# Performance work log

Hardware: AMD Instinct MI355X
Metric: run time of the kernel (lower is better)

Reference implementation:

```python
import jax, jax.numpy as jnp
import numpy as np
from jax import lax

D_MODEL = 768
D_INNER = 1536   # expand * d_model
D_STATE = 16
D_CONV = 4
DT_RANK = 48     # ceil(768/16)
BATCH, SEQLEN = 2, 1024


def silu(x):
    return x * jax.nn.sigmoid(x)


def causal_conv1d(x, w, b):
    # x: (B, L, d)  w: (d, K) depthwise  b: (d,)
    # matches torch Conv1d(groups=d, padding=K-1)[..., :L]
    K = w.shape[1]
    L = x.shape[1]
    xp = jnp.pad(x, ((0, 0), (K - 1, 0), (0, 0)))
    out = b
    for k in range(K):
        out = out + xp[:, k:k + L, :] * w[:, k]
    return out


def mamba_branch(xz, conv_w, conv_b, x_proj_w, dt_proj_w, dt_bias, A_log, D):
    # xz: (B, L, 2*d_inner); faithful to mamba_inner_fn_no_out_proj
    x, z = jnp.split(xz, 2, axis=-1)
    x = silu(causal_conv1d(x, conv_w, conv_b))
    x_dbl = x @ x_proj_w.T                                  # (B,L,dt_rank+2N)
    dt, Bc, Cc = jnp.split(x_dbl, [DT_RANK, DT_RANK + D_STATE], axis=-1)
    delta = jax.nn.softplus(dt @ dt_proj_w.T + dt_bias)     # (B,L,d)
    A = -jnp.exp(A_log)                                     # (d,N)
    dA = jnp.exp(delta[..., None] * A)                      # (B,L,d,N)
    dBx = (delta * x)[..., None] * Bc[:, :, None, :]        # (B,L,d,N)

    def step(h, inp):
        da, dbx = inp
        h = da * h + dbx
        return h, h

    h0 = jnp.zeros((x.shape[0], x.shape[2], D_STATE), x.dtype)
    _, hs = lax.scan(step, h0, (jnp.swapaxes(dA, 0, 1), jnp.swapaxes(dBx, 0, 1)))
    y = jnp.einsum('lbdn,bln->bld', hs, Cc) + x * D         # (B,L,d)
    return y * silu(z)


def setup_inputs() -> dict:
    key = jax.random.key(0)
    ks = jax.random.split(key, 16)
    d, dm, n, r, K = D_INNER, D_MODEL, D_STATE, DT_RANK, D_CONV
    A_log = jnp.log(jnp.broadcast_to(jnp.arange(1, n + 1, dtype=jnp.float32), (d, n)))
    # faithful dt bias init: inverse-softplus of log-uniform dt in [1e-3, 1e-1]
    def dt_bias(k):
        dt = jnp.exp(jax.random.uniform(k, (d,)) * (np.log(0.1) - np.log(0.001)) + np.log(0.001))
        dt = jnp.clip(dt, 1e-4)
        return dt + jnp.log(-jnp.expm1(-dt))
    return {
        'hidden_states': jax.random.normal(ks[0], (BATCH, SEQLEN, dm), jnp.float32),
        'in_proj_w': jax.random.normal(ks[1], (2 * d, dm), jnp.float32) / np.sqrt(dm),
        'conv_w': jax.random.normal(ks[2], (d, K), jnp.float32) / np.sqrt(K),
        'conv_b': jax.random.normal(ks[3], (d,), jnp.float32) * 0.02,
        'x_proj_w': jax.random.normal(ks[4], (r + 2 * n, d), jnp.float32) / np.sqrt(d),
        'dt_proj_w': jax.random.uniform(ks[5], (d, r), jnp.float32, -r ** -0.5, r ** -0.5),
        'dt_proj_b': dt_bias(ks[6]),
        'A_log': A_log,
        'D': jnp.ones((d,), jnp.float32),
        'conv_w_b': jax.random.normal(ks[7], (d, K), jnp.float32) / np.sqrt(K),
        'conv_b_b': jax.random.normal(ks[8], (d,), jnp.float32) * 0.02,
        'x_proj_w_b': jax.random.normal(ks[9], (r + 2 * n, d), jnp.float32) / np.sqrt(d),
        'dt_proj_w_b': jax.random.uniform(ks[10], (d, r), jnp.float32, -r ** -0.5, r ** -0.5),
        'dt_proj_b_b': dt_bias(ks[11]),
        'A_b_log': A_log,
        'D_b': jnp.ones((d,), jnp.float32),
        'out_proj_w': jax.random.normal(ks[12], (dm, d), jnp.float32) / np.sqrt(d),
    }


def reference(hidden_states, in_proj_w, conv_w, conv_b, x_proj_w, dt_proj_w, dt_proj_b,
              A_log, D, conv_w_b, conv_b_b, x_proj_w_b, dt_proj_w_b, dt_proj_b_b,
              A_b_log, D_b, out_proj_w):
    # bimamba v2: forward scan + backward (flipped) scan, summed, then out_proj
    xz = hidden_states @ in_proj_w.T                        # (B,L,2*d_inner)
    out_f = mamba_branch(xz, conv_w, conv_b, x_proj_w, dt_proj_w, dt_proj_b, A_log, D)
    out_r = mamba_branch(xz[:, ::-1, :], conv_w_b, conv_b_b, x_proj_w_b,
                         dt_proj_w_b, dt_proj_b_b, A_b_log, D_b)[:, ::-1, :]
    return (out_f + out_r) @ out_proj_w.T                   # (B,L,d_model)
```

## Files before the change

### kernel.cpp

```cpp
#include <hip/hip_runtime.h>
#include <hip/hip_bf16.h>

#define LL 1024
#define DI 1536
#define N2 3072
#define ML 2048

typedef __attribute__((ext_vector_type(8))) short short8;
typedef __attribute__((ext_vector_type(4))) float f4;
typedef __attribute__((ext_vector_type(4))) float f32x4;

__device__ __forceinline__ ushort f2bf(float f) {
  union { float f; unsigned u; } v; v.f = f;
  unsigned u = v.u;
  u += 0x7fffu + ((u >> 16) & 1u);
  return (ushort)(u >> 16);
}
__device__ __forceinline__ float bf2f(ushort u) {
  union { unsigned i; float f; } w; w.i = ((unsigned)u) << 16; return w.f;
}
__device__ __forceinline__ f4 bf2f4(ushort4 u) {
  f4 r; r.x = bf2f(u.x); r.y = bf2f(u.y); r.z = bf2f(u.z); r.w = bf2f(u.w);
  return r;
}

__device__ __forceinline__ void gload16(const ushort* g, ushort* l) {
  __builtin_amdgcn_global_load_lds(
      (const __attribute__((address_space(1))) unsigned int*)g,
      (__attribute__((address_space(3))) unsigned int*)l, 16, 0, 0);
}

struct CvtSeg { const float* s; ushort* d; int n4; };
struct Cvt5 { CvtSeg seg[5]; };

#define CVT_BLOCKS 5232

__global__ void k_cvt(Cvt5 p, int total4,
                      const float* __restrict__ wf, const float* __restrict__ wb,
                      ushort* __restrict__ dtw) {
  int bid = blockIdx.x;
  if (bid < CVT_BLOCKS) {
    int i = bid * 256 + threadIdx.x;
    if (i >= total4) return;
    int off = i, sidx = 0;
    while (sidx < 4 && off >= p.seg[sidx].n4) { off -= p.seg[sidx].n4; ++sidx; }
    f4 v = *(const f4*)(p.seg[sidx].s + (size_t)off * 4);
    ushort4 o;
    o.x = f2bf(v.x); o.y = f2bf(v.y); o.z = f2bf(v.z); o.w = f2bf(v.w);
    *(ushort4*)(p.seg[sidx].d + (size_t)off * 4) = o;
  } else {
    int i = (bid - CVT_BLOCKS) * 256 + threadIdx.x;
    int c = i & 63;
    int rr = i >> 6;
    int dir = rr / 1536;
    int r = rr - dir * 1536;
    const float* w = dir ? wb : wf;
    dtw[i] = (c < 48) ? f2bf(w[r * 48 + c]) : (ushort)0;
  }
}

template<int EPI, bool NGUARD, int KS, bool OBF>
__global__ __launch_bounds__(256)
void k_gemm(const ushort* __restrict__ A, const ushort* __restrict__ Bm,
            void* __restrict__ Cp, int M, int N, int K,
            const float* __restrict__ bias, const float* __restrict__ bias2,
            size_t sA, size_t sB, size_t sC, size_t sKs, int kLen) {
  const int dir = blockIdx.z;
  A += (size_t)dir * sA;
  Bm += (size_t)dir * sB;
  size_t cbase = (size_t)dir * sC;
  const float* bp = (EPI == 1) ? (dir ? bias2 : bias) : nullptr;

  int n0, kOff, kEnd;
  if (KS > 1) {
    int yb_ = blockIdx.y;
    int nt = yb_ / KS, ks = yb_ - nt * KS;
    n0 = nt * 128;
    kOff = ks * kLen;
    kEnd = kOff + kLen;
    cbase += (size_t)ks * sKs;
  } else {
    n0 = blockIdx.y * 128;
    kOff = 0;
    kEnd = K;
  }

  __shared__ ushort As[128 * 32];
  __shared__ ushort Bs[128 * 32];
  const int tid = threadIdx.x;
  const int m0 = blockIdx.x * 128;
  const int wv = tid >> 6;
  const int lane = tid & 63;
  const int wr = (wv >> 1) * 64;
  const int wc = (wv & 1) * 64;
  const int lr = lane & 15;
  const int lk = lane >> 4;
  f32x4 acc[4][4] = {};
  for (int k0 = kOff; k0 < kEnd; k0 += 32) {
    #pragma unroll
    for (int i = 0; i < 2; ++i) {
      int e = (tid + i * 256) * 8;
      int r = e >> 5;
      int c = e & 31;
      gload16(A + (size_t)(m0 + r) * K + k0 + c, &As[(i * 256 + wv * 64) * 8]);
      gload16(Bm + (size_t)(n0 + r) * K + k0 + c, &Bs[(i * 256 + wv * 64) * 8]);
    }
    __syncthreads();
    short8 af[4], bfr[4];
    #pragma unroll
    for (int m = 0; m < 4; ++m) af[m] = *(const short8*)(&As[(wr + m*16 + lr) * 32 + lk*8]);
    #pragma unroll
    for (int n = 0; n < 4; ++n) bfr[n] = *(const short8*)(&Bs[(wc + n*16 + lr) * 32 + lk*8]);
    #pragma unroll
    for (int m = 0; m < 4; ++m)
      #pragma unroll
      for (int n = 0; n < 4; ++n)
        acc[m][n] = __builtin_amdgcn_mfma_f32_16x16x32_bf16(af[m], bfr[n], acc[m][n], 0, 0, 0);
    __syncthreads();
  }
  #pragma unroll
  for (int m = 0; m < 4; ++m) {
    int gr = m0 + wr + m * 16 + lk * 4;
    #pragma unroll
    for (int n = 0; n < 4; ++n) {
      int gc = n0 + wc + n * 16 + lr;
      if (NGUARD && gc >= N) continue;
      #pragma unroll
      for (int r = 0; r < 4; ++r) {
        float v = acc[m][n][r];
        if (EPI == 1) {
          v += bp[gc];
          v = (v > 20.f) ? v : log1pf(__expf(v));
        }
        size_t idx = cbase + (size_t)(gr + r) * N + gc;
        if (OBF) ((ushort*)Cp)[idx] = f2bf(v);
        else     ((float*)Cp)[idx] = v;
      }
    }
  }
}

__global__ void k_xred(const float* __restrict__ partial,
                       float* __restrict__ dtBC, ushort* __restrict__ dtbf) {
  int i = blockIdx.x * 256 + threadIdx.x;
  int dir = i / 40960;
  int rem = i - dir * 40960;
  int row = rem / 20;
  int c4 = rem - row * 20;
  f4 s = {0.f, 0.f, 0.f, 0.f};
  #pragma unroll
  for (int ks = 0; ks < 8; ++ks) {
    f4 v = *(const f4*)(partial + (((size_t)(dir * 8 + ks) * 2048 + row) * 80 + c4 * 4));
    s.x += v.x; s.y += v.y; s.z += v.z; s.w += v.w;
  }
  *(f4*)(dtBC + ((size_t)dir * 163840 + (size_t)row * 80 + c4 * 4)) = s;
  if (c4 < 16) {
    ushort4 u;
    if (c4 < 12) { u.x = f2bf(s.x); u.y = f2bf(s.y); u.z = f2bf(s.z); u.w = f2bf(s.w); }
    else { u.x = 0; u.y = 0; u.z = 0; u.w = 0; }
    *(ushort4*)(dtbf + ((size_t)dir * 131072 + (size_t)row * 64 + c4 * 4)) = u;
  }
}

__global__ void k_ored(const float* __restrict__ part, float* __restrict__ out) {
  int i = blockIdx.x * 256 + threadIdx.x;
  f4 s = {0.f, 0.f, 0.f, 0.f};
  #pragma unroll
  for (int ks = 0; ks < 4; ++ks) {
    f4 v = *(const f4*)(part + (size_t)ks * 1572864 + (size_t)i * 4);
    s.x += v.x; s.y += v.y; s.z += v.z; s.w += v.w;
  }
  *(f4*)(out + (size_t)i * 4) = s;
}

#define CONV_R 8
__global__ __launch_bounds__(192)
void k_conv2(const ushort* __restrict__ xz,
             const float* __restrict__ wf, const float* __restrict__ bf_,
             const float* __restrict__ wb, const float* __restrict__ bb_,
             ushort* __restrict__ xcbf) {
  int d4 = blockIdx.z * 192 + threadIdx.x;
  int b = blockIdx.y;
  int l0 = blockIdx.x * CONV_R;
  int d = d4 * 4;
  f4 w0[4], w1[4];
  #pragma unroll
  for (int c = 0; c < 4; ++c) {
    w0[c] = *(const f4*)(wf + (size_t)d * 4 + c * 4);
    w1[c] = *(const f4*)(wb + (size_t)d * 4 + c * 4);
  }
  f4 bias0 = *(const f4*)(bf_ + d);
  f4 bias1 = *(const f4*)(bb_ + d);
  f4 win[CONV_R + 6];
  #pragma unroll
  for (int j = 0; j < CONV_R + 6; ++j) {
    int t = l0 - 3 + j;
    if (t >= 0 && t < LL) {
      win[j] = bf2f4(*(const ushort4*)(xz + ((size_t)(b * LL + t)) * N2 + d));
    } else {
      f4 z = {0.f, 0.f, 0.f, 0.f};
      win[j] = z;
    }
  }
  #pragma unroll
  for (int i = 0; i < CONV_R; ++i) {
    int l = l0 + i;
    float a0[4], a1[4];
    #pragma unroll
    for (int c = 0; c < 4; ++c) { a0[c] = bias0[c]; a1[c] = bias1[c]; }
    #pragma unroll
    for (int k = 0; k < 4; ++k) {
      f4 xv0 = win[i + k];
      f4 xv1 = win[i + 3 + k];
      #pragma unroll
      for (int c = 0; c < 4; ++c) {
        a0[c] += xv0[c] * w0[c][k];
        a1[c] += xv1[c] * w1[c][3 - k];
      }
    }
    ushort4 o0, o1;
    #pragma unroll
    for (int c = 0; c < 4; ++c) {
      a0[c] = a0[c] / (1.f + __expf(-a0[c]));
      a1[c] = a1[c] / (1.f + __expf(-a1[c]));
    }
    o0.x = f2bf(a0[0]); o0.y = f2bf(a0[1]); o0.z = f2bf(a0[2]); o0.w = f2bf(a0[3]);
    o1.x = f2bf(a1[0]); o1.y = f2bf(a1[1]); o1.z = f2bf(a1[2]); o1.w = f2bf(a1[3]);
    *(ushort4*)(xcbf + ((size_t)(b * LL + l)) * DI + d) = o0;
    *(ushort4*)(xcbf + ((size_t)(ML + b * LL + (LL - 1 - l))) * DI + d) = o1;
  }
}

__global__ __launch_bounds__(256)
void k_scan1(const ushort* __restrict__ delta_all,
             const ushort* __restrict__ xc_all,
             const float* __restrict__ dtBC_all,
             const float* __restrict__ Alog_f, const float* __restrict__ Alog_b,
             float* __restrict__ hL, float* __restrict__ P) {
  int dirb = blockIdx.z;
  int dir = dirb >> 1, b = dirb & 1;
  int ch = blockIdx.y;
  int tid = threadIdx.x;
  int lane = tid & 63;
  int wv = tid >> 6;
  int ns = lane >> 4;
  int dl_ = lane & 15;
  int d = blockIdx.x * 64 + wv * 16 + dl_;
  const float* Alog = dir ? Alog_b : Alog_f;
  float Av[4];
  #pragma unroll
  for (int j = 0; j < 4; ++j) Av[j] = -__expf(Alog[d * 16 + ns * 4 + j]);
  int l0 = ch * 64;
  size_t base = ((size_t)dir * ML + (size_t)b * LL + l0) * DI + d;
  const ushort* dptr = delta_all + base;
  const ushort* xptr = xc_all + base;
  const float* bc = dtBC_all + ((size_t)dir * ML + (size_t)b * LL + l0) * 80 + 48 + ns * 4;
  float h[4] = {0.f, 0.f, 0.f, 0.f};
  float s = 0.f;
  #pragma unroll 4
  for (int l = 0; l < 64; ++l) {
    float dl = bf2f(dptr[(size_t)l * DI]);
    float xv = bf2f(xptr[(size_t)l * DI]);
    f4 Bv = *(const f4*)(bc + l * 80);
    float dbx = dl * xv;
    s += dl;
    #pragma unroll
    for (int j = 0; j < 4; ++j) {
      float dA = __expf(dl * Av[j]);
      h[j] = dA * h[j] + dbx * Bv[j];
    }
  }
  size_t si = (((size_t)dirb * 1536 + d) * 16 + ch) * 16 + ns * 4;
  f4 hv = {h[0], h[1], h[2], h[3]};
  f4 pv = {__expf(Av[0] * s), __expf(Av[1] * s), __expf(Av[2] * s), __expf(Av[3] * s)};
  *(f4*)(hL + si) = hv;
  *(f4*)(P + si) = pv;
}

__global__ void k_comb(const float* __restrict__ hL, const float* __restrict__ P,
                       float* __restrict__ hIn) {
  int tid = blockIdx.x * 256 + threadIdx.x;
  int n = tid & 15;
  size_t c = tid >> 4;
  float h = 0.f;
  size_t base = c * 256 + n;
  #pragma unroll
  for (int ch = 0; ch < 16; ++ch) {
    hIn[base + ch * 16] = h;
    h = P[base + ch * 16] * h + hL[base + ch * 16];
  }
}

__global__ __launch_bounds__(256)
void k_scan2(const ushort* __restrict__ delta_all,
             const ushort* __restrict__ xc_all,
             const float* __restrict__ dtBC_all,
             const float* __restrict__ Alog_f, const float* __restrict__ Df,
             const float* __restrict__ Alog_b, const float* __restrict__ Db,
             const float* __restrict__ hIn,
             ushort* __restrict__ yf, ushort* __restrict__ yb) {
  int dirb = blockIdx.z;
  int dir = dirb >> 1, b = dirb & 1;
  int ch = blockIdx.y;
  int tid = threadIdx.x;
  int lane = tid & 63;
  int wv = tid >> 6;
  int ns = lane >> 4;
  int dl_ = lane & 15;
  int d = blockIdx.x * 64 + wv * 16 + dl_;
  const float* Alog = dir ? Alog_b : Alog_f;
  const float* Dp = dir ? Db : Df;
  float Av[4];
  #pragma unroll
  for (int j = 0; j < 4; ++j) Av[j] = -__expf(Alog[d * 16 + ns * 4 + j]);
  float Dvv = Dp[d];
  int l0 = ch * 64;
  size_t base = ((size_t)dir * ML + (size_t)b * LL + l0) * DI + d;
  const ushort* dptr = delta_all + base;
  const ushort* xptr = xc_all + base;
  const float* bc = dtBC_all + ((size_t)dir * ML + (size_t)b * LL + l0) * 80 + 48 + ns * 4;
  ushort* yo = dir ? yb : yf;
  size_t hi = (((size_t)dirb * 1536 + d) * 16 + ch) * 16 + ns * 4;
  f4 h0 = *(const f4*)(hIn + hi);
  float h[4] = {h0.x, h0.y, h0.z, h0.w};
  #pragma unroll 4
  for (int l = 0; l < 64; ++l) {
    float dl = bf2f(dptr[(size_t)l * DI]);
    float xv = bf2f(xptr[(size_t)l * DI]);
    f4 Bv = *(const f4*)(bc + l * 80);
    f4 Cv = *(const f4*)(bc + 16 + l * 80);
    float dbx = dl * xv;
    float pr = 0.f;
    #pragma unroll
    for (int j = 0; j < 4; ++j) {
      float dA = __expf(dl * Av[j]);
      h[j] = dA * h[j] + dbx * Bv[j];
      pr += h[j] * Cv[j];
    }
    pr += __shfl_xor(pr, 16);
    pr += __shfl_xor(pr, 32);
    if (ns == 0) {
      int gl = l0 + l;
      int lo = dir ? (LL - 1 - gl) : gl;
      yo[((size_t)b * LL + lo) * DI + d] = f2bf(pr + xv * Dvv);
    }
  }
}

__global__ void k_gate(const ushort* __restrict__ a, const ushort* __restrict__ b,
                       const ushort* __restrict__ xz, ushort* __restrict__ o) {
  int i = blockIdx.x * 256 + threadIdx.x;
  int row = i / 384;
  int c4 = i - row * 384;
  f4 va = bf2f4(*(const ushort4*)(a + (size_t)i * 4));
  f4 vb = bf2f4(*(const ushort4*)(b + (size_t)i * 4));
  f4 vz = bf2f4(*(const ushort4*)(xz + (size_t)row * N2 + DI + c4 * 4));
  ushort4 u;
  float s0 = vz.x / (1.f + __expf(-vz.x));
  float s1 = vz.y / (1.f + __expf(-vz.y));
  float s2 = vz.z / (1.f + __expf(-vz.z));
  float s3 = vz.w / (1.f + __expf(-vz.w));
  u.x = f2bf((va.x + vb.x) * s0);
  u.y = f2bf((va.y + vb.y) * s1);
  u.z = f2bf((va.z + vb.z) * s2);
  u.w = f2bf((va.w + vb.w) * s3);
  *(ushort4*)(o + (size_t)i * 4) = u;
}

extern "C" void kernel_launch(void* const* d_in, const int* in_sizes, int n_in,
                              void* d_out, int out_size, void* d_ws, size_t ws_size,
                              hipStream_t stream) {
  const float* hidden      = (const float*)d_in[0];
  const float* in_proj_w   = (const float*)d_in[1];
  const float* conv_w      = (const float*)d_in[2];
  const float* conv_b      = (const float*)d_in[3];
  const float* x_proj_w    = (const float*)d_in[4];
  const float* dt_proj_w   = (const float*)d_in[5];
  const float* dt_proj_b   = (const float*)d_in[6];
  const float* A_log       = (const float*)d_in[7];
  const float* Dv          = (const float*)d_in[8];
  const float* conv_w_b    = (const float*)d_in[9];
  const float* conv_b_b    = (const float*)d_in[10];
  const float* x_proj_w_b  = (const float*)d_in[11];
  const float* dt_proj_w_b = (const float*)d_in[12];
  const float* dt_proj_b_b = (const float*)d_in[13];
  const float* A_b_log     = (const float*)d_in[14];
  const float* D_b         = (const float*)d_in[15];
  const float* out_proj_w  = (const float*)d_in[16];
  float* out = (float*)d_out;

  float* wsf   = (float*)d_ws;
  float* dtBC  = wsf;
  float* hL    = wsf + 327680;
  float* P     = wsf + 1900544;
  float* hIn   = wsf + 3473408;
  float* xpart = wsf + 327680;
  float* opart = wsf;
  ushort* wsb      = (ushort*)((char*)d_ws + 25165824);
  ushort* hid_bf   = wsb;
  ushort* win_bf   = wsb + 1572864;
  ushort* xw_bf    = wsb + 3932160;
  ushort* dtw_bf   = wsb + 4177920;
  ushort* wout_bf  = wsb + 4374528;
  ushort* xz_bf    = wsb + 5554176;
  ushort* xc_bf    = wsb + 11845632;
  ushort* dt_bf    = wsb + 18137088;
  ushort* delta_bf = wsb + 18399232;
  ushort* ybf_f    = wsb + 24690688;
  ushort* ybf_b    = wsb + 27836416;
  ushort* y_bf     = wsb + 30982144;
  if (ws_size < 93421568) return;

  Cvt5 c5;
  c5.seg[0] = { hidden,      hid_bf,            1572864 / 4 };
  c5.seg[1] = { in_proj_w,   win_bf,            2359296 / 4 };
  c5.seg[2] = { x_proj_w,    xw_bf,             122880 / 4 };
  c5.seg[3] = { x_proj_w_b,  xw_bf + 122880,    122880 / 4 };
  c5.seg[4] = { out_proj_w,  wout_bf,           1179648 / 4 };
  k_cvt<<<CVT_BLOCKS + 768, 256, 0, stream>>>(c5, 1339392, dt_proj_w, dt_proj_w_b, dtw_bf);

  k_gemm<0, false, 1, true><<<dim3(16, 24), 256, 0, stream>>>(
      hid_bf, win_bf, xz_bf, 2048, 3072, 768, nullptr, nullptr, 0, 0, 0, 0, 0);

  k_conv2<<<dim3(LL / CONV_R, 2, 2), 192, 0, stream>>>(
      xz_bf, conv_w, conv_b, conv_w_b, conv_b_b, xc_bf);

  k_gemm<0, true, 8, false><<<dim3(16, 8, 2), 256, 0, stream>>>(
      xc_bf, xw_bf, xpart, 2048, 80, 1536, nullptr, nullptr,
      3145728, 122880, 1310720, 163840, 192);
  k_xred<<<320, 256, 0, stream>>>(xpart, dtBC, dt_bf);

  k_gemm<1, false, 1, true><<<dim3(16, 12, 2), 256, 0, stream>>>(
      dt_bf, dtw_bf, delta_bf, 2048, 1536, 64, dt_proj_b, dt_proj_b_b,
      131072, 98304, 3145728, 0, 0);

  k_scan1<<<dim3(24, 16, 4), 256, 0, stream>>>(delta_bf, xc_bf, dtBC, A_log, A_b_log, hL, P);
  k_comb<<<384, 256, 0, stream>>>(hL, P, hIn);
  k_scan2<<<dim3(24, 16, 4), 256, 0, stream>>>(delta_bf, xc_bf, dtBC,
                                               A_log, Dv, A_b_log, D_b, hIn, ybf_f, ybf_b);

  k_gate<<<3072, 256, 0, stream>>>(ybf_f, ybf_b, xz_bf, y_bf);

  k_gemm<0, false, 4, false><<<dim3(16, 24), 256, 0, stream>>>(
      y_bf, wout_bf, opart, 2048, 768, 1536, nullptr, nullptr,
      0, 0, 0, 1572864, 384);
  k_ored<<<1536, 256, 0, stream>>>(opart, out);
}
```

Before: 277.2 us.

## Give each scan thread all 16 states of one channel, use 32-step chunks

The chunked selective scan now maps one thread to one channel holding all 16 state values, in place of four lanes each holding four states and combining with shuffles. The sequence is split into 32 chunks of 32 steps, and the hL/P/hIn buffers are relaid out channel-contiguous per chunk, with the combine kernel rewritten to match. This drops the cross-lane shuffle reduction and the predicated store, and lets each channel's delta and x values be loaded by a single thread. The cost is more registers per thread, fewer threads per chunk (6x32x4 blocks), and a larger workspace.

```diff
diff --git a/kernel.cpp b/kernel.cpp
--- a/kernel.cpp
+++ b/kernel.cpp
@@ -240,54 +240,58 @@
   int dirb = blockIdx.z;
   int dir = dirb >> 1, b = dirb & 1;
   int ch = blockIdx.y;
-  int tid = threadIdx.x;
-  int lane = tid & 63;
-  int wv = tid >> 6;
-  int ns = lane >> 4;
-  int dl_ = lane & 15;
-  int d = blockIdx.x * 64 + wv * 16 + dl_;
+  int d = blockIdx.x * 256 + threadIdx.x;
   const float* Alog = dir ? Alog_b : Alog_f;
-  float Av[4];
-  #pragma unroll
-  for (int j = 0; j < 4; ++j) Av[j] = -__expf(Alog[d * 16 + ns * 4 + j]);
-  int l0 = ch * 64;
+  float Av[16];
+  #pragma unroll
+  for (int n = 0; n < 16; ++n) Av[n] = -__expf(Alog[d * 16 + n]);
+  int l0 = ch * 32;
   size_t base = ((size_t)dir * ML + (size_t)b * LL + l0) * DI + d;
   const ushort* dptr = delta_all + base;
   const ushort* xptr = xc_all + base;
-  const float* bc = dtBC_all + ((size_t)dir * ML + (size_t)b * LL + l0) * 80 + 48 + ns * 4;
-  float h[4] = {0.f, 0.f, 0.f, 0.f};
+  const float* bc = dtBC_all + ((size_t)dir * ML + (size_t)b * LL + l0) * 80 + 48;
+  float h[16];
+  #pragma unroll
+  for (int n = 0; n < 16; ++n) h[n] = 0.f;
   float s = 0.f;
-  #pragma unroll 4
-  for (int l = 0; l < 64; ++l) {
+  for (int l = 0; l < 32; ++l) {
     float dl = bf2f(dptr[(size_t)l * DI]);
     float xv = bf2f(xptr[(size_t)l * DI]);
-    f4 Bv = *(const f4*)(bc + l * 80);
     float dbx = dl * xv;
     s += dl;
-    #pragma unroll
-    for (int j = 0; j < 4; ++j) {
-      float dA = __expf(dl * Av[j]);
-      h[j] = dA * h[j] + dbx * Bv[j];
-    }
-  }
-  size_t si = (((size_t)dirb * 1536 + d) * 16 + ch) * 16 + ns * 4;
-  f4 hv = {h[0], h[1], h[2], h[3]};
-  f4 pv = {__expf(Av[0] * s), __expf(Av[1] * s), __expf(Av[2] * s), __expf(Av[3] * s)};
-  *(f4*)(hL + si) = hv;
-  *(f4*)(P + si) = pv;
+    const float* bp = bc + l * 80;
+    #pragma unroll
+    for (int q = 0; q < 4; ++q) {
+      f4 Bv = *(const f4*)(bp + q * 4);
+      #pragma unroll
+      for (int j = 0; j < 4; ++j) {
+        int n = q * 4 + j;
+        h[n] = __expf(dl * Av[n]) * h[n] + dbx * Bv[j];
+      }
+    }
+  }
+  size_t si = (((size_t)dirb * 32 + ch) * 1536 + d) * 16;
+  #pragma unroll
+  for (int q = 0; q < 4; ++q) {
+    f4 hv = {h[q*4], h[q*4+1], h[q*4+2], h[q*4+3]};
+    f4 pv = {__expf(Av[q*4] * s), __expf(Av[q*4+1] * s),
+             __expf(Av[q*4+2] * s), __expf(Av[q*4+3] * s)};
+    *(f4*)(hL + si + q * 4) = hv;
+    *(f4*)(P + si + q * 4) = pv;
+  }
 }
 
 __global__ void k_comb(const float* __restrict__ hL, const float* __restrict__ P,
                        float* __restrict__ hIn) {
   int tid = blockIdx.x * 256 + threadIdx.x;
-  int n = tid & 15;
-  size_t c = tid >> 4;
+  int dirb = tid / 24576;
+  int e = tid - dirb * 24576;
+  size_t base = (size_t)dirb * 786432 + e;
   float h = 0.f;
-  size_t base = c * 256 + n;
-  #pragma unroll
-  for (int ch = 0; ch < 16; ++ch) {
-    hIn[base + ch * 16] = h;
-    h = P[base + ch * 16] * h + hL[base + ch * 16];
+  #pragma unroll
+  for (int ch = 0; ch < 32; ++ch) {
+    hIn[base + (size_t)ch * 24576] = h;
+    h = P[base + (size_t)ch * 24576] * h + hL[base + (size_t)ch * 24576];
   }
 }
 
@@ -302,48 +306,50 @@
   int dirb = blockIdx.z;
   int dir = dirb >> 1, b = dirb & 1;
   int ch = blockIdx.y;
-  int tid = threadIdx.x;
-  int lane = tid & 63;
-  int wv = tid >> 6;
-  int ns = lane >> 4;
-  int dl_ = lane & 15;
-  int d = blockIdx.x * 64 + wv * 16 + dl_;
+  int d = blockIdx.x * 256 + threadIdx.x;
   const float* Alog = dir ? Alog_b : Alog_f;
   const float* Dp = dir ? Db : Df;
-  float Av[4];
-  #pragma unroll
-  for (int j = 0; j < 4; ++j) Av[j] = -__expf(Alog[d * 16 + ns * 4 + j]);
+  float Av[16];
+  #pragma unroll
+  for (int n = 0; n < 16; ++n) Av[n] = -__expf(Alog[d * 16 + n]);
   float Dvv = Dp[d];
-  int l0 = ch * 64;
+  int l0 = ch * 32;
   size_t base = ((size_t)dir * ML + (size_t)b * LL + l0) * DI + d;
   const ushort* dptr = delta_all + base;
   const ushort* xptr = xc_all + base;
-  const float* bc = dtBC_all + ((size_t)dir * ML + (size_t)b * LL + l0) * 80 + 48 + ns * 4;
+  const float* bc = dtBC_all + ((size_t)dir * ML + (size_t)b * LL + l0) * 80 + 48;
   ushort* yo = dir ? yb : yf;
-  size_t hi = (((size_t)dirb * 1536 + d) * 16 + ch) * 16 + ns * 4;
-  f4 h0 = *(const f4*)(hIn + hi);
-  float h[4] = {h0.x, h0.y, h0.z, h0.w};
-  #pragma unroll 4
-  for (int l = 0; l < 64; ++l) {
+  size_t si = (((size_t)dirb * 32 + ch) * 1536 + d) * 16;
+  float h[16];
+  #pragma unroll
+  for (int q = 0; q < 4; ++q) {
+    f4 hv = *(const f4*)(hIn + si + q * 4);
+    h[q*4] = hv.x; h[q*4+1] = hv.y; h[q*4+2] = hv.z; h[q*4+3] = hv.w;
+  }
+  for (int l = 0; l < 32; ++l) {
     float dl = bf2f(dptr[(size_t)l * DI]);
     float xv = bf2f(xptr[(size_t)l * DI]);
-    f4 Bv = *(const f4*)(bc + l * 80);
-    f4 Cv = *(const f4*)(bc + 16 + l * 80);
     float dbx = dl * xv;
-    float pr = 0.f;
-    #pragma unroll
-    for (int j = 0; j < 4; ++j) {
-      float dA = __expf(dl * Av[j]);
-      h[j] = dA * h[j] + dbx * Bv[j];
-      pr += h[j] * Cv[j];
-    }
-    pr += __shfl_xor(pr, 16);
-    pr += __shfl_xor(pr, 32);
-    if (ns == 0) {
-      int gl = l0 + l;
-      int lo = dir ? (LL - 1 - gl) : gl;
-      yo[((size_t)b * LL + lo) * DI + d] = f2bf(pr + xv * Dvv);
-    }
+    const float* bp = bc + l * 80;
+    float pr0 = 0.f, pr1 = 0.f, pr2 = 0.f, pr3 = 0.f;
+    #pragma unroll
+    for (int q = 0; q < 4; ++q) {
+      f4 Bv = *(const f4*)(bp + q * 4);
+      f4 Cv = *(const f4*)(bp + 16 + q * 4);
+      float pq = 0.f;
+      #pragma unroll
+      for (int j = 0; j < 4; ++j) {
+        int n = q * 4 + j;
+        h[n] = __expf(dl * Av[n]) * h[n] + dbx * Bv[j];
+        pq += h[n] * Cv[j];
+      }
+      if (q == 0) pr0 = pq; else if (q == 1) pr1 = pq;
+      else if (q == 2) pr2 = pq; else pr3 = pq;
+    }
+    float pr = (pr0 + pr1) + (pr2 + pr3);
+    int gl = l0 + l;
+    int lo = dir ? (LL - 1 - gl) : gl;
+    yo[((size_t)b * LL + lo) * DI + d] = f2bf(pr + xv * Dvv);
   }
 }
 
@@ -392,11 +398,11 @@
   float* wsf   = (float*)d_ws;
   float* dtBC  = wsf;
   float* hL    = wsf + 327680;
-  float* P     = wsf + 1900544;
-  float* hIn   = wsf + 3473408;
+  float* P     = wsf + 3473408;
+  float* hIn   = wsf + 6619136;
   float* xpart = wsf + 327680;
-  float* opart = wsf;
-  ushort* wsb      = (ushort*)((char*)d_ws + 25165824);
+  float* opart = wsf + 327680;
+  ushort* wsb      = (ushort*)((char*)d_ws + 39059456);
   ushort* hid_bf   = wsb;
   ushort* win_bf   = wsb + 1572864;
   ushort* xw_bf    = wsb + 3932160;
@@ -409,7 +415,7 @@
   ushort* ybf_f    = wsb + 24690688;
   ushort* ybf_b    = wsb + 27836416;
   ushort* y_bf     = wsb + 30982144;
-  if (ws_size < 93421568) return;
+  if (ws_size < 107315200) return;
 
   Cvt5 c5;
   c5.seg[0] = { hidden,      hid_bf,            1572864 / 4 };
@@ -434,10 +440,10 @@
       dt_bf, dtw_bf, delta_bf, 2048, 1536, 64, dt_proj_b, dt_proj_b_b,
       131072, 98304, 3145728, 0, 0);
 
-  k_scan1<<<dim3(24, 16, 4), 256, 0, stream>>>(delta_bf, xc_bf, dtBC, A_log, A_b_log, hL, P);
+  k_scan1<<<dim3(6, 32, 4), 256, 0, stream>>>(delta_bf, xc_bf, dtBC, A_log, A_b_log, hL, P);
   k_comb<<<384, 256, 0, stream>>>(hL, P, hIn);
-  k_scan2<<<dim3(24, 16, 4), 256, 0, stream>>>(delta_bf, xc_bf, dtBC,
-                                               A_log, Dv, A_b_log, D_b, hIn, ybf_f, ybf_b);
+  k_scan2<<<dim3(6, 32, 4), 256, 0, stream>>>(delta_bf, xc_bf, dtBC,
+                                              A_log, Dv, A_b_log, D_b, hIn, ybf_f, ybf_b);
 
   k_gate<<<3072, 256, 0, stream>>>(ybf_f, ybf_b, xz_bf, y_bf);
 
```

Measured after the change: 278.2 us. No clear change (+0.4%).
